# Kernel tuning notes

Measured on AMD Instinct MI355X. Metric: run time of the kernel, lower is better.

## Reference

```python
import jax, jax.numpy as jnp
import numpy as np

B, S = 64, 1000
ENC, DEC = 512, 512


def setup_inputs() -> dict:
    key = jax.random.key(0)
    k1, k2, k3, k4, k5 = jax.random.split(key, 5)
    hidden = jax.random.normal(k1, (B, DEC), dtype=jnp.float32)
    encoder_outputs = jax.random.normal(k2, (B, S, 2 * ENC), dtype=jnp.float32)
    # attn: Linear(enc_hidden_dim*2 + dec_hidden_dim -> dec_hidden_dim)
    fan_in = 2 * ENC + DEC
    bound = 1.0 / np.sqrt(fan_in)
    attn_w = jax.random.uniform(k3, (fan_in, DEC), minval=-bound, maxval=bound, dtype=jnp.float32)
    attn_b = jax.random.uniform(k4, (DEC,), minval=-bound, maxval=bound, dtype=jnp.float32)
    v = jax.random.uniform(k5, (DEC,), dtype=jnp.float32)  # torch.rand -> U[0,1)
    return {"hidden": hidden, "encoder_outputs": encoder_outputs,
            "attn_w": attn_w, "attn_b": attn_b, "v": v}


def reference(hidden, encoder_outputs, attn_w, attn_b, v):
    # hidden: [B, D], encoder_outputs: [B, S, 2E]
    S_len = encoder_outputs.shape[1]
    h_rep = jnp.broadcast_to(hidden[:, None, :], (hidden.shape[0], S_len, hidden.shape[1]))
    cat = jnp.concatenate([h_rep, encoder_outputs], axis=2)          # [B, S, D+2E]
    energy = jnp.tanh(cat @ attn_w + attn_b)                          # [B, S, D]
    attention = jnp.einsum('bsd,d->bs', energy, v)                    # [B, S]
    return jax.nn.softmax(attention, axis=1)
```

## Files before the change

kernel.cpp:

```cpp
#include <hip/hip_runtime.h>
#include <hip/hip_bf16.h>

typedef __attribute__((ext_vector_type(8))) short short8;
typedef __attribute__((ext_vector_type(4))) float float4v;

__device__ inline unsigned short f2bf(float f) {
    union { float f; unsigned int i; } c; c.f = f;
    unsigned int r = c.i + 0x7FFFu + ((c.i >> 16) & 1u);
    return (unsigned short)(r >> 16);
}

__global__ void k_transpose(const float* __restrict__ W,
                            unsigned short* __restrict__ Wt) {
    int idx = blockIdx.x * 256 + threadIdx.x;
    int d  = idx & 511;
    int kg = idx >> 9;
    short8 v;
#pragma unroll
    for (int j = 0; j < 8; j++)
        v[j] = (short)f2bf(W[(size_t)(512 + kg * 8 + j) * 512 + d]);
    *(short8*)(Wt + (size_t)d * 1024 + kg * 8) = v;
}

__global__ void k_hb(const float* __restrict__ hidden,
                     const float* __restrict__ W,
                     const float* __restrict__ bias,
                     float* __restrict__ hb) {
    int b = blockIdx.x, d = threadIdx.x;
    __shared__ float h[512];
    h[d] = hidden[b * 512 + d];
    __syncthreads();
    float a = 0.f;
#pragma unroll 8
    for (int k = 0; k < 512; k++)
        a += h[k] * W[(size_t)k * 512 + d];
    hb[b * 512 + d] = a + bias[d];
}

__launch_bounds__(256, 2)
__global__ void k_main(const float* __restrict__ enc,
                       const unsigned short* __restrict__ Wt,
                       const float* __restrict__ hb,
                       const float* __restrict__ vvec,
                       float* __restrict__ att) {
    const int b    = blockIdx.y;
    const int s0   = blockIdx.x * 64;
    const int tid  = threadIdx.x;
    const int wave = tid >> 6;
    const int lane = tid & 63;
    const int col  = lane & 15;
    const int quad = lane >> 4;

    __shared__ unsigned short As[2][64][72];

    const int r  = tid >> 2;
    const int cq = tid & 3;
    int s = s0 + r; if (s > 999) s = 999;
    const float* arow = enc + ((size_t)(b * 1000 + s) * 1024 + cq * 16);

    const unsigned short* bptr = Wt + (size_t)(wave * 128 + col) * 1024 + quad * 8;

    float4v acc[4][8];
#pragma unroll
    for (int mt = 0; mt < 4; mt++)
#pragma unroll
        for (int nt = 0; nt < 8; nt++)
            acc[mt][nt] = float4v{0.f, 0.f, 0.f, 0.f};

    float4v st[4];
#pragma unroll
    for (int j = 0; j < 4; j++) st[j] = *(const float4v*)(arow + j * 4);
    {
        short8 wv0, wv1;
#pragma unroll
        for (int j = 0; j < 4; j++) {
            wv0[j]     = (short)f2bf(st[0][j]);
            wv0[j + 4] = (short)f2bf(st[1][j]);
            wv1[j]     = (short)f2bf(st[2][j]);
            wv1[j + 4] = (short)f2bf(st[3][j]);
        }
        unsigned short* wp = &As[0][r][cq * 16];
        *(short8*)(wp)     = wv0;
        *(short8*)(wp + 8) = wv1;
    }
    __syncthreads();

    for (int c = 0; c < 16; c++) {
        const int buf = c & 1;

        if (c < 15) {
#pragma unroll
            for (int j = 0; j < 4; j++)
                st[j] = *(const float4v*)(arow + (c + 1) * 64 + j * 4);
        }

        short8 af[2][4];
#pragma unroll
        for (int ks = 0; ks < 2; ks++)
#pragma unroll
            for (int mt = 0; mt < 4; mt++)
                af[ks][mt] = *(const short8*)(&As[buf][mt * 16 + col][ks * 32 + quad * 8]);

#pragma unroll
        for (int ks = 0; ks < 2; ks++) {
            short8 bf[8];
#pragma unroll
            for (int nt = 0; nt < 8; nt++)
                bf[nt] = *(const short8*)(bptr + c * 64 + ks * 32 + (size_t)nt * 16 * 1024);
#pragma unroll
            for (int mt = 0; mt < 4; mt++)
#pragma unroll
                for (int nt = 0; nt < 8; nt++)
                    acc[mt][nt] = __builtin_amdgcn_mfma_f32_16x16x32_bf16(
                        af[ks][mt], bf[nt], acc[mt][nt], 0, 0, 0);
        }

        if (c < 15) {
            short8 wv0, wv1;
#pragma unroll
            for (int j = 0; j < 4; j++) {
                wv0[j]     = (short)f2bf(st[0][j]);
                wv0[j + 4] = (short)f2bf(st[1][j]);
                wv1[j]     = (short)f2bf(st[2][j]);
                wv1[j + 4] = (short)f2bf(st[3][j]);
            }
            unsigned short* wq = &As[buf ^ 1][r][cq * 16];
            *(short8*)(wq)     = wv0;
            *(short8*)(wq + 8) = wv1;
        }
        __syncthreads();
    }

    float vv[8], hbv[8];
#pragma unroll
    for (int nt = 0; nt < 8; nt++) {
        int d = wave * 128 + nt * 16 + col;
        vv[nt]  = vvec[d];
        hbv[nt] = hb[b * 512 + d];
    }
    float rs[4][4];
#pragma unroll
    for (int mt = 0; mt < 4; mt++)
#pragma unroll
        for (int rg = 0; rg < 4; rg++) rs[mt][rg] = 0.f;

#pragma unroll
    for (int mt = 0; mt < 4; mt++)
#pragma unroll
        for (int nt = 0; nt < 8; nt++)
#pragma unroll
            for (int rg = 0; rg < 4; rg++) {
                float e = acc[mt][nt][rg] + hbv[nt];
                float t = 1.f - 2.f / (__expf(2.f * e) + 1.f);
                rs[mt][rg] += t * vv[nt];
            }

#pragma unroll
    for (int mt = 0; mt < 4; mt++)
#pragma unroll
        for (int rg = 0; rg < 4; rg++) {
            float x = rs[mt][rg];
            x += __shfl_xor(x, 1);
            x += __shfl_xor(x, 2);
            x += __shfl_xor(x, 4);
            x += __shfl_xor(x, 8);
            rs[mt][rg] = x;
        }

    __shared__ float red[4][64];
    if (col == 0) {
#pragma unroll
        for (int mt = 0; mt < 4; mt++)
#pragma unroll
            for (int rg = 0; rg < 4; rg++)
                red[wave][mt * 16 + quad * 4 + rg] = rs[mt][rg];
    }
    __syncthreads();
    if (tid < 64) {
        float sum = red[0][tid] + red[1][tid] + red[2][tid] + red[3][tid];
        int ss = s0 + tid;
        if (ss < 1000) att[b * 1000 + ss] = sum;
    }
}

__global__ void k_softmax(const float* __restrict__ att,
                          float* __restrict__ out) {
    int b = blockIdx.x, tid = threadIdx.x;
    __shared__ float sm[4], ss[4];
    float x[4], mx = -1e30f;
#pragma unroll
    for (int i = 0; i < 4; i++) {
        int s = tid + 256 * i;
        x[i] = (s < 1000) ? att[b * 1000 + s] : -1e30f;
        mx = fmaxf(mx, x[i]);
    }
    for (int off = 1; off < 64; off <<= 1) mx = fmaxf(mx, __shfl_xor(mx, off));
    if ((tid & 63) == 0) sm[tid >> 6] = mx;
    __syncthreads();
    mx = fmaxf(fmaxf(sm[0], sm[1]), fmaxf(sm[2], sm[3]));

    float ex[4], se = 0.f;
#pragma unroll
    for (int i = 0; i < 4; i++) {
        ex[i] = __expf(x[i] - mx);
        if (tid + 256 * i >= 1000) ex[i] = 0.f;
        se += ex[i];
    }
    for (int off = 1; off < 64; off <<= 1) se += __shfl_xor(se, off);
    if ((tid & 63) == 0) ss[tid >> 6] = se;
    __syncthreads();
    se = ss[0] + ss[1] + ss[2] + ss[3];
    float inv = 1.f / se;
#pragma unroll
    for (int i = 0; i < 4; i++) {
        int s = tid + 256 * i;
        if (s < 1000) out[b * 1000 + s] = ex[i] * inv;
    }
}

extern "C" void kernel_launch(void* const* d_in, const int* in_sizes, int n_in,
                              void* d_out, int out_size, void* d_ws, size_t ws_size,
                              hipStream_t stream) {
    const float* hidden = (const float*)d_in[0];
    const float* enc    = (const float*)d_in[1];
    const float* attn_w = (const float*)d_in[2];
    const float* attn_b = (const float*)d_in[3];
    const float* v      = (const float*)d_in[4];
    float* out = (float*)d_out;

    char* ws = (char*)d_ws;
    unsigned short* Wt = (unsigned short*)ws;
    float* hb  = (float*)(ws + (1 << 20));
    float* att = (float*)(ws + (1 << 20) + (128 << 10));

    k_transpose<<<256, 256, 0, stream>>>(attn_w, Wt);
    k_hb<<<64, 512, 0, stream>>>(hidden, attn_w, attn_b, hb);
    k_main<<<dim3(16, 64), 256, 0, stream>>>(enc, Wt, hb, v, att);
    k_softmax<<<64, 256, 0, stream>>>(att, out);
}
```

Measured before the change: 481.3 us.

## Use 8 waves per block in main GEMM with register-prefetched W and two-stage A prefetch

The main kernel now runs 512 threads (8 waves), so each wave covers 64 output columns instead of 128, which halves the accumulators per wave. W fragments are double-buffered in registers and loaded one chunk ahead. Encoder rows are prefetched two chunks ahead, with each thread loading 8 floats. The hb kernel is split across 4 column groups to spread it over more blocks. This adds latency hiding and parallelism at the cost of more register pressure from the prefetch buffers and a larger cross-wave reduction.

New measurement: 487.2 us. Within noise of the previous version (+1.2%).

```diff
diff --git a/kernel.cpp b/kernel.cpp
--- a/kernel.cpp
+++ b/kernel.cpp
@@ -26,18 +26,19 @@
                      const float* __restrict__ W,
                      const float* __restrict__ bias,
                      float* __restrict__ hb) {
-    int b = blockIdx.x, d = threadIdx.x;
+    int b = blockIdx.y, dg = blockIdx.x, tid = threadIdx.x;
+    int d = dg * 128 + tid;
     __shared__ float h[512];
-    h[d] = hidden[b * 512 + d];
+    for (int k = tid; k < 512; k += 128) h[k] = hidden[b * 512 + k];
     __syncthreads();
     float a = 0.f;
-#pragma unroll 8
+#pragma unroll 16
     for (int k = 0; k < 512; k++)
         a += h[k] * W[(size_t)k * 512 + d];
     hb[b * 512 + d] = a + bias[d];
 }
 
-__launch_bounds__(256, 2)
+__launch_bounds__(512, 2)
 __global__ void k_main(const float* __restrict__ enc,
                        const unsigned short* __restrict__ Wt,
                        const float* __restrict__ hb,
@@ -52,46 +53,57 @@
     const int quad = lane >> 4;
 
     __shared__ unsigned short As[2][64][72];
-
-    const int r  = tid >> 2;
-    const int cq = tid & 3;
+    __shared__ float red[8][64];
+
+    const int r   = tid >> 3;
+    const int seg = tid & 7;
     int s = s0 + r; if (s > 999) s = 999;
-    const float* arow = enc + ((size_t)(b * 1000 + s) * 1024 + cq * 16);
-
-    const unsigned short* bptr = Wt + (size_t)(wave * 128 + col) * 1024 + quad * 8;
-
-    float4v acc[4][8];
-#pragma unroll
-    for (int mt = 0; mt < 4; mt++)
-#pragma unroll
-        for (int nt = 0; nt < 8; nt++)
+    const float* arow = enc + ((size_t)(b * 1000 + s) * 1024) + seg * 8;
+
+    const unsigned short* bbase = Wt + (size_t)(wave * 64 + col) * 1024 + quad * 8;
+
+    float4v acc[4][4];
+#pragma unroll
+    for (int mt = 0; mt < 4; mt++)
+#pragma unroll
+        for (int nt = 0; nt < 4; nt++)
             acc[mt][nt] = float4v{0.f, 0.f, 0.f, 0.f};
 
-    float4v st[4];
-#pragma unroll
-    for (int j = 0; j < 4; j++) st[j] = *(const float4v*)(arow + j * 4);
+    short8  bf[2][8];
+    float4v sp[2][2];
+
     {
-        short8 wv0, wv1;
-#pragma unroll
-        for (int j = 0; j < 4; j++) {
-            wv0[j]     = (short)f2bf(st[0][j]);
-            wv0[j + 4] = (short)f2bf(st[1][j]);
-            wv1[j]     = (short)f2bf(st[2][j]);
-            wv1[j + 4] = (short)f2bf(st[3][j]);
-        }
-        unsigned short* wp = &As[0][r][cq * 16];
-        *(short8*)(wp)     = wv0;
-        *(short8*)(wp + 8) = wv1;
-    }
-    __syncthreads();
-
+        float4v a0 = *(const float4v*)(arow);
+        float4v a1 = *(const float4v*)(arow + 4);
+        short8 wv;
+#pragma unroll
+        for (int j = 0; j < 4; j++) { wv[j] = (short)f2bf(a0[j]); wv[j + 4] = (short)f2bf(a1[j]); }
+        *(short8*)&As[0][r][seg * 8] = wv;
+    }
+    sp[0][0] = *(const float4v*)(arow + 64);
+    sp[0][1] = *(const float4v*)(arow + 68);
+#pragma unroll
+    for (int nt = 0; nt < 4; nt++)
+#pragma unroll
+        for (int ks = 0; ks < 2; ks++)
+            bf[0][nt * 2 + ks] = *(const short8*)(bbase + (size_t)nt * 16384 + ks * 32);
+    __syncthreads();
+
+#pragma unroll
     for (int c = 0; c < 16; c++) {
-        const int buf = c & 1;
+        const int cur = c & 1, nxt = cur ^ 1;
 
         if (c < 15) {
 #pragma unroll
-            for (int j = 0; j < 4; j++)
-                st[j] = *(const float4v*)(arow + (c + 1) * 64 + j * 4);
+            for (int nt = 0; nt < 4; nt++)
+#pragma unroll
+                for (int ks = 0; ks < 2; ks++)
+                    bf[nxt][nt * 2 + ks] =
+                        *(const short8*)(bbase + (size_t)nt * 16384 + (c + 1) * 64 + ks * 32);
+        }
+        if (c < 14) {
+            sp[nxt][0] = *(const float4v*)(arow + (c + 2) * 64);
+            sp[nxt][1] = *(const float4v*)(arow + (c + 2) * 64 + 4);
         }
 
         short8 af[2][4];
@@ -99,42 +111,33 @@
         for (int ks = 0; ks < 2; ks++)
 #pragma unroll
             for (int mt = 0; mt < 4; mt++)
-                af[ks][mt] = *(const short8*)(&As[buf][mt * 16 + col][ks * 32 + quad * 8]);
-
-#pragma unroll
-        for (int ks = 0; ks < 2; ks++) {
-            short8 bf[8];
-#pragma unroll
-            for (int nt = 0; nt < 8; nt++)
-                bf[nt] = *(const short8*)(bptr + c * 64 + ks * 32 + (size_t)nt * 16 * 1024);
+                af[ks][mt] = *(const short8*)&As[cur][mt * 16 + col][ks * 32 + quad * 8];
+
+#pragma unroll
+        for (int ks = 0; ks < 2; ks++)
 #pragma unroll
             for (int mt = 0; mt < 4; mt++)
 #pragma unroll
-                for (int nt = 0; nt < 8; nt++)
+                for (int nt = 0; nt < 4; nt++)
                     acc[mt][nt] = __builtin_amdgcn_mfma_f32_16x16x32_bf16(
-                        af[ks][mt], bf[nt], acc[mt][nt], 0, 0, 0);
-        }
+                        af[ks][mt], bf[cur][nt * 2 + ks], acc[mt][nt], 0, 0, 0);
 
         if (c < 15) {
-            short8 wv0, wv1;
+            short8 wv;
 #pragma unroll
             for (int j = 0; j < 4; j++) {
-                wv0[j]     = (short)f2bf(st[0][j]);
-                wv0[j + 4] = (short)f2bf(st[1][j]);
-                wv1[j]     = (short)f2bf(st[2][j]);
-                wv1[j + 4] = (short)f2bf(st[3][j]);
+                wv[j]     = (short)f2bf(sp[cur][0][j]);
+                wv[j + 4] = (short)f2bf(sp[cur][1][j]);
             }
-            unsigned short* wq = &As[buf ^ 1][r][cq * 16];
-            *(short8*)(wq)     = wv0;
-            *(short8*)(wq + 8) = wv1;
+            *(short8*)&As[nxt][r][seg * 8] = wv;
         }
         __syncthreads();
     }
 
-    float vv[8], hbv[8];
-#pragma unroll
-    for (int nt = 0; nt < 8; nt++) {
-        int d = wave * 128 + nt * 16 + col;
+    float vv[4], hbv[4];
+#pragma unroll
+    for (int nt = 0; nt < 4; nt++) {
+        int d = wave * 64 + nt * 16 + col;
         vv[nt]  = vvec[d];
         hbv[nt] = hb[b * 512 + d];
     }
@@ -147,7 +150,7 @@
 #pragma unroll
     for (int mt = 0; mt < 4; mt++)
 #pragma unroll
-        for (int nt = 0; nt < 8; nt++)
+        for (int nt = 0; nt < 4; nt++)
 #pragma unroll
             for (int rg = 0; rg < 4; rg++) {
                 float e = acc[mt][nt][rg] + hbv[nt];
@@ -167,7 +170,6 @@
             rs[mt][rg] = x;
         }
 
-    __shared__ float red[4][64];
     if (col == 0) {
 #pragma unroll
         for (int mt = 0; mt < 4; mt++)
@@ -177,7 +179,8 @@
     }
     __syncthreads();
     if (tid < 64) {
-        float sum = red[0][tid] + red[1][tid] + red[2][tid] + red[3][tid];
+        float sum = red[0][tid] + red[1][tid] + red[2][tid] + red[3][tid]
+                  + red[4][tid] + red[5][tid] + red[6][tid] + red[7][tid];
         int ss = s0 + tid;
         if (ss < 1000) att[b * 1000 + ss] = sum;
     }
@@ -234,7 +237,7 @@
     float* att = (float*)(ws + (1 << 20) + (128 << 10));
 
     k_transpose<<<256, 256, 0, stream>>>(attn_w, Wt);
-    k_hb<<<64, 512, 0, stream>>>(hidden, attn_w, attn_b, hb);
-    k_main<<<dim3(16, 64), 256, 0, stream>>>(enc, Wt, hb, v, att);
+    k_hb<<<dim3(4, 64), 128, 0, stream>>>(hidden, attn_w, attn_b, hb);
+    k_main<<<dim3(16, 64), 512, 0, stream>>>(enc, Wt, hb, v, att);
     k_softmax<<<64, 256, 0, stream>>>(att, out);
 }
```
